# Kernel optimization log

Measured on AMD Instinct MI355X. Metric: run time of the kernel, lower is better.

Reference implementation:

```python
import jax, jax.numpy as jnp
import numpy as np

NODE_DIM = 128
OUT_DIM = 64
N_NODES = 50000
N_EDGES = 800000
NEG_SLOPE = 0.01  # F.leaky_relu default


def setup_inputs() -> dict:
    key = jax.random.key(0)
    k1, k2, k3, k4, k5 = jax.random.split(key, 5)
    h = jax.random.normal(k1, (N_NODES, NODE_DIM), dtype=jnp.float32)
    src = jax.random.randint(k2, (N_EDGES,), 0, N_NODES, dtype=jnp.int32)
    dst = jax.random.randint(k3, (N_EDGES,), 0, N_NODES, dtype=jnp.int32)
    # fc: Linear(node_dim, out_dim, bias=False); attn_fc: Linear(2*out_dim, 1, bias=False)
    W_fc = jax.random.normal(k4, (NODE_DIM, OUT_DIM), dtype=jnp.float32) * (1.0 / np.sqrt(NODE_DIM))
    W_attn = jax.random.normal(k5, (2 * OUT_DIM, 1), dtype=jnp.float32) * (1.0 / np.sqrt(2 * OUT_DIM))
    return {"h": h, "src": src, "dst": dst, "W_fc": W_fc, "W_attn": W_attn}


def reference(h, src, dst, W_fc, W_attn):
    N = h.shape[0]
    D = W_fc.shape[1]
    z = h @ W_fc                                   # [N, D]
    # attn_fc(concat(z_src, z_dst)) == z_src @ Wa[:D] + z_dst @ Wa[D:]
    s_src = (z @ W_attn[:D]).squeeze(-1)            # [N]
    s_dst = (z @ W_attn[D:]).squeeze(-1)            # [N]
    e = jax.nn.leaky_relu(s_src[src] + s_dst[dst], NEG_SLOPE)  # [E]
    # segment softmax over incoming edges per dst node
    m = jax.ops.segment_max(e, dst, num_segments=N)            # [N]
    ex = jnp.exp(e - m[dst])                                   # [E]
    denom = jax.ops.segment_sum(ex, dst, num_segments=N)       # [N]
    alpha = ex / denom[dst]                                    # [E]
    # weighted scatter-sum of src features into dst nodes
    out = jax.ops.segment_sum(alpha[:, None] * z[src], dst, num_segments=N)  # [N, D]
    return out
```

## Files before the change

kernel.cpp:

```cpp
#include <hip/hip_runtime.h>

#define NODE_DIM 128
#define OUT_DIM  64
#define NEG_SLOPE 0.01f
#define EPB   4096
#define CAPC  64
#define MAXB  4800

typedef __attribute__((ext_vector_type(8))) short short8;
typedef __attribute__((ext_vector_type(4))) short short4v;
typedef __attribute__((ext_vector_type(4))) float float4e;

__device__ __forceinline__ unsigned short f2bf(float f) {
    unsigned u = __float_as_uint(f);
    unsigned r = (u + 0x7FFFu + ((u >> 16) & 1u)) >> 16;
    return (unsigned short)r;
}
__device__ __forceinline__ float bf2f(unsigned short v) {
    return __uint_as_float((unsigned)v << 16);
}
__device__ __forceinline__ void split_bf(float v, short& hi, short& lo) {
    unsigned short h = f2bf(v);
    float r = v - bf2f(h);
    hi = (short)h;
    lo = (short)f2bf(r);
}

__global__ __launch_bounds__(256) void k_proj_part(
    const float* __restrict__ h, const float* __restrict__ Wf,
    const float* __restrict__ Wa,
    unsigned short* __restrict__ zbf,
    float* __restrict__ s_src, float* __restrict__ s_dst,
    const int* __restrict__ src, const int* __restrict__ dst,
    int* __restrict__ chunks, int* __restrict__ bhist,
    int N, int E, int PB, int nblkP)
{
    if (blockIdx.x >= (unsigned)PB) {
        __shared__ int cnt[256];
        const int blk = blockIdx.x - PB;
        const int t = threadIdx.x;
        cnt[t] = 0;
        __syncthreads();
        const int e0 = blk * EPB + t * 16;
        if (e0 < E) {
            int ne = E - e0; if (ne > 16) ne = 16;
            if (ne == 16) {
                int db[16], sb[16];
                const int4* dp = (const int4*)(dst + e0);
                const int4* sp = (const int4*)(src + e0);
                #pragma unroll
                for (int q = 0; q < 4; ++q) {
                    int4 dv = dp[q], svv = sp[q];
                    db[q*4+0]=dv.x; db[q*4+1]=dv.y; db[q*4+2]=dv.z; db[q*4+3]=dv.w;
                    sb[q*4+0]=svv.x; sb[q*4+1]=svv.y; sb[q*4+2]=svv.z; sb[q*4+3]=svv.w;
                }
                #pragma unroll
                for (int k = 0; k < 16; ++k) {
                    int d = db[k];
                    int bk = d >> 8;
                    int r = atomicAdd(&cnt[bk], 1);
                    if (r < CAPC)
                        chunks[((size_t)bk * nblkP + blk) * CAPC + r] = ((d & 255) << 17) | sb[k];
                }
            } else {
                for (int k = 0; k < ne; ++k) {
                    int d = dst[e0 + k];
                    int bk = d >> 8;
                    int r = atomicAdd(&cnt[bk], 1);
                    if (r < CAPC)
                        chunks[((size_t)bk * nblkP + blk) * CAPC + r] = ((d & 255) << 17) | src[e0 + k];
                }
            }
        }
        __syncthreads();
        bhist[t * nblkP + blk] = (cnt[t] < CAPC) ? cnt[t] : CAPC;
        return;
    }
    const int t    = threadIdx.x;
    const int wv   = t >> 6;
    const int lane = t & 63;
    const int m    = lane & 15;
    const int quad = lane >> 4;
    const int row0 = blockIdx.x * 64 + wv * 16;

    int rowc = row0 + m; if (rowc > N - 1) rowc = N - 1;
    const float* hrow = h + (size_t)rowc * NODE_DIM;
    short8 Ahi[4], Alo[4];
    #pragma unroll
    for (int t4 = 0; t4 < 4; ++t4) {
        float4e v0 = *(const float4e*)(hrow + t4 * 32 + quad * 8);
        float4e v1 = *(const float4e*)(hrow + t4 * 32 + quad * 8 + 4);
        #pragma unroll
        for (int j = 0; j < 4; ++j) {
            short hi, lo;
            split_bf(v0[j], hi, lo);
            Ahi[t4][j] = hi; Alo[t4][j] = lo;
            split_bf(v1[j], hi, lo);
            Ahi[t4][4 + j] = hi; Alo[t4][4 + j] = lo;
        }
    }

    float ps[4] = {0.f, 0.f, 0.f, 0.f};
    float pd[4] = {0.f, 0.f, 0.f, 0.f};

    #pragma unroll
    for (int c = 0; c < 4; ++c) {
        float4e acc = {0.f, 0.f, 0.f, 0.f};
        int col = c * 16 + m;
        #pragma unroll
        for (int t4 = 0; t4 < 4; ++t4) {
            short8 bh, bl;
            #pragma unroll
            for (int j = 0; j < 8; ++j) {
                short hi, lo;
                split_bf(Wf[(t4 * 32 + quad * 8 + j) * OUT_DIM + col], hi, lo);
                bh[j] = hi; bl[j] = lo;
            }
            acc = __builtin_amdgcn_mfma_f32_16x16x32_bf16(Alo[t4], bh, acc, 0, 0, 0);
            acc = __builtin_amdgcn_mfma_f32_16x16x32_bf16(Ahi[t4], bl, acc, 0, 0, 0);
            acc = __builtin_amdgcn_mfma_f32_16x16x32_bf16(Ahi[t4], bh, acc, 0, 0, 0);
        }
        float was = Wa[col];
        float wad = Wa[OUT_DIM + col];
        #pragma unroll
        for (int r = 0; r < 4; ++r) {
            int nrow = row0 + quad * 4 + r;
            if (nrow < N) zbf[(size_t)nrow * OUT_DIM + col] = f2bf(acc[r]);
            ps[r] = fmaf(acc[r], was, ps[r]);
            pd[r] = fmaf(acc[r], wad, pd[r]);
        }
    }

    #pragma unroll
    for (int r = 0; r < 4; ++r) {
        #pragma unroll
        for (int off = 1; off < 16; off <<= 1) {
            ps[r] += __shfl_xor(ps[r], off, 64);
            pd[r] += __shfl_xor(pd[r], off, 64);
        }
    }
    if (m == 0) {
        #pragma unroll
        for (int r = 0; r < 4; ++r) {
            int nrow = row0 + quad * 4 + r;
            if (nrow < N) { s_src[nrow] = ps[r]; s_dst[nrow] = pd[r]; }
        }
    }
}

__global__ __launch_bounds__(1024) void k_bucket_agg(
    const int* __restrict__ chunks, const int* __restrict__ bhist,
    const float* __restrict__ s_src, const float* __restrict__ s_dst,
    const unsigned short* __restrict__ zbf,
    float* __restrict__ out, int N, int nblkP)
{
    __shared__ int soff[257];
    __shared__ int sU[MAXB];
    __shared__ int sSrc[MAXB];
    __shared__ float xs[MAXB];
    __shared__ int cntN[256], curN[256], rsN[256], sscan[256];
    const int b = blockIdx.x;
    const int t = threadIdx.x;

    int v = 0;
    if (t < 256) {
        v = (t < nblkP) ? bhist[b * nblkP + t] : 0;
        sscan[t] = v;
        cntN[t] = 0;
    }
    __syncthreads();
    #pragma unroll
    for (int off = 1; off < 256; off <<= 1) {
        int u = 0;
        if (t < 256 && t >= off) u = sscan[t - off];
        __syncthreads();
        if (t < 256) sscan[t] += u;
        __syncthreads();
    }
    if (t < 256) soff[t] = sscan[t] - v;
    if (t == 255) soff[256] = sscan[255];
    __syncthreads();
    int total = soff[256];
    if (total > MAXB) total = MAXB;

    for (int i = t; i < total; i += 1024) {
        int lo = 0, hi = nblkP;
        while (hi - lo > 1) {
            int mid = (lo + hi) >> 1;
            if (soff[mid] <= i) lo = mid; else hi = mid;
        }
        int val = chunks[((size_t)b * nblkP + lo) * CAPC + (i - soff[lo])];
        sU[i] = val;
        atomicAdd(&cntN[val >> 17], 1);
    }
    __syncthreads();
    int vc = 0;
    if (t < 256) { vc = cntN[t]; sscan[t] = vc; }
    __syncthreads();
    #pragma unroll
    for (int off = 1; off < 256; off <<= 1) {
        int u = 0;
        if (t < 256 && t >= off) u = sscan[t - off];
        __syncthreads();
        if (t < 256) sscan[t] += u;
        __syncthreads();
    }
    if (t < 256) { rsN[t] = sscan[t] - vc; curN[t] = sscan[t] - vc; }
    __syncthreads();
    const int nodeBase = b * 256;
    for (int i = t; i < total; i += 1024) {
        int val = sU[i];
        int n8 = val >> 17;
        int sidx = val & 0x1FFFF;
        int pos = atomicAdd(&curN[n8], 1);
        sSrc[pos] = sidx;
        float e = s_src[sidx] + s_dst[nodeBase + n8];
        e = (e > 0.f) ? e : e * NEG_SLOPE;
        xs[pos] = __expf(e);
    }
    __syncthreads();

    const int wid = t >> 6, lane = t & 63;
    const int quad = lane >> 4, col4 = (lane & 15) * 4;
    for (int k = 0; k < 16; ++k) {
        int n8 = wid * 16 + k;
        int node = nodeBase + n8;
        if (node >= N) continue;
        int rs = rsN[n8], dg = cntN[n8];
        if (dg == 0) {
            if (quad == 0) {
                float4e o = {0.f, 0.f, 0.f, 0.f};
                *(float4e*)(out + (size_t)node * OUT_DIM + col4) = o;
            }
            continue;
        }
        float a0 = 0.f, a1 = 0.f, a2 = 0.f, a3 = 0.f, den = 0.f;
        for (int base = 0; base < dg; base += 64)
            if (lane < dg - base) den += xs[rs + base + lane];
        for (int j = 0; j < dg; j += 16) {
            #pragma unroll
            for (int g = 0; g < 4; ++g) {
                int ei = j + g * 4 + quad;
                int idx = rs + ((ei < dg) ? ei : 0);
                int ss = sSrc[idx];
                float xx = (ei < dg) ? xs[idx] : 0.f;
                short4v zv = *(const short4v*)(zbf + ((unsigned)ss << 6) + col4);
                a0 = fmaf(xx, bf2f((unsigned short)zv[0]), a0);
                a1 = fmaf(xx, bf2f((unsigned short)zv[1]), a1);
                a2 = fmaf(xx, bf2f((unsigned short)zv[2]), a2);
                a3 = fmaf(xx, bf2f((unsigned short)zv[3]), a3);
            }
        }
        a0 += __shfl_xor(a0, 16, 64); a0 += __shfl_xor(a0, 32, 64);
        a1 += __shfl_xor(a1, 16, 64); a1 += __shfl_xor(a1, 32, 64);
        a2 += __shfl_xor(a2, 16, 64); a2 += __shfl_xor(a2, 32, 64);
        a3 += __shfl_xor(a3, 16, 64); a3 += __shfl_xor(a3, 32, 64);
        #pragma unroll
        for (int off = 32; off > 0; off >>= 1) den += __shfl_xor(den, off, 64);
        if (quad == 0) {
            float4e o;
            o[0] = a0 / den; o[1] = a1 / den; o[2] = a2 / den; o[3] = a3 / den;
            *(float4e*)(out + (size_t)node * OUT_DIM + col4) = o;
        }
    }
}

extern "C" void kernel_launch(void* const* d_in, const int* in_sizes, int n_in,
                              void* d_out, int out_size, void* d_ws, size_t ws_size,
                              hipStream_t stream) {
    const float* h   = (const float*)d_in[0];
    const int*   src = (const int*)d_in[1];
    const int*   dst = (const int*)d_in[2];
    const float* Wf  = (const float*)d_in[3];
    const float* Wa  = (const float*)d_in[4];
    const int N = in_sizes[0] / NODE_DIM;
    const int E = in_sizes[1];
    float* out = (float*)d_out;

    const int PB    = (N + 63) / 64;
    const int nblkP = (E + EPB - 1) / EPB;
    const int nbB   = (N + 255) / 256;

    char* ws = (char*)d_ws;
    size_t off = 0;
    int* chunks = (int*)(ws + off);             off += (size_t)256 * nblkP * CAPC * sizeof(int);
    int* bhist  = (int*)(ws + off);             off += (size_t)256 * nblkP * sizeof(int);
    unsigned short* zbf = (unsigned short*)(ws + off); off += (size_t)N * OUT_DIM * sizeof(unsigned short);
    float* s_src = (float*)(ws + off);          off += (size_t)N * sizeof(float);
    float* s_dst = (float*)(ws + off);          off += (size_t)N * sizeof(float);

    k_proj_part<<<PB + nblkP, 256, 0, stream>>>(h, Wf, Wa, zbf, s_src, s_dst,
                                                src, dst, chunks, bhist, N, E, PB, nblkP);
    k_bucket_agg<<<nbB, 1024, 0, stream>>>(chunks, bhist, s_src, s_dst, zbf, out, N, nblkP);
}
```

Measured before the change: 133.2 us.

## Stage W split in LDS, coalesce z stores, restructure bucket aggregation

The projection kernel now splits W_fc into bf16 hi/lo parts once per block in shared memory, instead of having every wave reload and resplit it from global memory. It also stages z tiles through LDS so that global stores are coalesced 16-byte rows rather than scattered 2-byte writes. The aggregation kernel drops the binary-search compaction into sU and reads chunks directly per wave twice. It also assigns one node per 16-lane group, so each group walks its edges serially with 4-way unrolling and no cross-quad shuffles, which risks load imbalance across high-degree nodes.

```diff
diff --git a/kernel.cpp b/kernel.cpp
--- a/kernel.cpp
+++ b/kernel.cpp
@@ -35,8 +35,13 @@
     int* __restrict__ chunks, int* __restrict__ bhist,
     int N, int E, int PB, int nblkP)
 {
+    __shared__ union {
+        short w[16384];
+        unsigned short zt[4][16][68];
+    } uni;
+    __shared__ int cnt[256];
+
     if (blockIdx.x >= (unsigned)PB) {
-        __shared__ int cnt[256];
         const int blk = blockIdx.x - PB;
         const int t = threadIdx.x;
         cnt[t] = 0;
@@ -76,6 +81,7 @@
         bhist[t * nblkP + blk] = (cnt[t] < CAPC) ? cnt[t] : CAPC;
         return;
     }
+
     const int t    = threadIdx.x;
     const int wv   = t >> 6;
     const int lane = t & 63;
@@ -83,6 +89,26 @@
     const int quad = lane >> 4;
     const int row0 = blockIdx.x * 64 + wv * 16;
 
+    {
+        short* wh = uni.w;
+        short* wl = uni.w + 8192;
+        for (int s = t; s < 1024; s += 256) {
+            int combo = s >> 6;
+            int ln    = s & 63;
+            int c = combo >> 2, t4 = combo & 3;
+            int col = c * 16 + (ln & 15);
+            int kq  = t4 * 32 + (ln >> 4) * 8;
+            #pragma unroll
+            for (int j = 0; j < 8; ++j) {
+                short hi, lo;
+                split_bf(Wf[(kq + j) * OUT_DIM + col], hi, lo);
+                wh[s * 8 + j] = hi;
+                wl[s * 8 + j] = lo;
+            }
+        }
+    }
+    __syncthreads();
+
     int rowc = row0 + m; if (rowc > N - 1) rowc = N - 1;
     const float* hrow = h + (size_t)rowc * NODE_DIM;
     short8 Ahi[4], Alo[4];
@@ -102,30 +128,28 @@
 
     float ps[4] = {0.f, 0.f, 0.f, 0.f};
     float pd[4] = {0.f, 0.f, 0.f, 0.f};
-
+    unsigned short z16[16];
+
+    const short* wh = uni.w;
+    const short* wl = uni.w + 8192;
     #pragma unroll
     for (int c = 0; c < 4; ++c) {
         float4e acc = {0.f, 0.f, 0.f, 0.f};
-        int col = c * 16 + m;
         #pragma unroll
         for (int t4 = 0; t4 < 4; ++t4) {
-            short8 bh, bl;
-            #pragma unroll
-            for (int j = 0; j < 8; ++j) {
-                short hi, lo;
-                split_bf(Wf[(t4 * 32 + quad * 8 + j) * OUT_DIM + col], hi, lo);
-                bh[j] = hi; bl[j] = lo;
-            }
+            int slot = (c * 4 + t4) * 64 + lane;
+            short8 bh = *(const short8*)(wh + slot * 8);
+            short8 bl = *(const short8*)(wl + slot * 8);
             acc = __builtin_amdgcn_mfma_f32_16x16x32_bf16(Alo[t4], bh, acc, 0, 0, 0);
             acc = __builtin_amdgcn_mfma_f32_16x16x32_bf16(Ahi[t4], bl, acc, 0, 0, 0);
             acc = __builtin_amdgcn_mfma_f32_16x16x32_bf16(Ahi[t4], bh, acc, 0, 0, 0);
         }
+        int col = c * 16 + m;
         float was = Wa[col];
         float wad = Wa[OUT_DIM + col];
         #pragma unroll
         for (int r = 0; r < 4; ++r) {
-            int nrow = row0 + quad * 4 + r;
-            if (nrow < N) zbf[(size_t)nrow * OUT_DIM + col] = f2bf(acc[r]);
+            z16[c * 4 + r] = f2bf(acc[r]);
             ps[r] = fmaf(acc[r], was, ps[r]);
             pd[r] = fmaf(acc[r], wad, pd[r]);
         }
@@ -144,6 +168,26 @@
         for (int r = 0; r < 4; ++r) {
             int nrow = row0 + quad * 4 + r;
             if (nrow < N) { s_src[nrow] = ps[r]; s_dst[nrow] = pd[r]; }
+        }
+    }
+
+    __syncthreads();
+    {
+        unsigned short (*zt)[68] = uni.zt[wv];
+        #pragma unroll
+        for (int c = 0; c < 4; ++c)
+            #pragma unroll
+            for (int r = 0; r < 4; ++r)
+                zt[quad * 4 + r][c * 16 + m] = z16[c * 4 + r];
+        short* zb = (short*)zbf;
+        #pragma unroll
+        for (int i = 0; i < 2; ++i) {
+            int r    = i * 8 + (lane >> 3);
+            int colb = (lane & 7) * 8;
+            short8 zz = *(const short8*)&zt[r][colb];
+            int grow = row0 + r;
+            if (grow < N)
+                *(short8*)(zb + (size_t)grow * OUT_DIM + colb) = zz;
         }
     }
 }
@@ -154,20 +198,28 @@
     const unsigned short* __restrict__ zbf,
     float* __restrict__ out, int N, int nblkP)
 {
-    __shared__ int soff[257];
-    __shared__ int sU[MAXB];
-    __shared__ int sSrc[MAXB];
+    __shared__ int   sSrc[MAXB];
     __shared__ float xs[MAXB];
-    __shared__ int cntN[256], curN[256], rsN[256], sscan[256];
+    __shared__ int cntN[256], rsN[256], curN[256], sscan[256];
     const int b = blockIdx.x;
     const int t = threadIdx.x;
-
-    int v = 0;
-    if (t < 256) {
-        v = (t < nblkP) ? bhist[b * nblkP + t] : 0;
-        sscan[t] = v;
-        cntN[t] = 0;
-    }
+    const int wid = t >> 6, lane = t & 63;
+    const int nodeBase = b * 256;
+
+    if (t < 256) cntN[t] = 0;
+    __syncthreads();
+
+    for (int c = wid; c < nblkP; c += 16) {
+        int cc = bhist[b * nblkP + c];
+        if (lane < cc) {
+            int val = chunks[((size_t)b * nblkP + c) * CAPC + lane];
+            atomicAdd(&cntN[val >> 17], 1);
+        }
+    }
+    __syncthreads();
+
+    int vc = 0;
+    if (t < 256) { vc = cntN[t]; sscan[t] = vc; }
     __syncthreads();
     #pragma unroll
     for (int off = 1; off < 256; off <<= 1) {
@@ -177,90 +229,79 @@
         if (t < 256) sscan[t] += u;
         __syncthreads();
     }
-    if (t < 256) soff[t] = sscan[t] - v;
-    if (t == 255) soff[256] = sscan[255];
-    __syncthreads();
-    int total = soff[256];
-    if (total > MAXB) total = MAXB;
-
-    for (int i = t; i < total; i += 1024) {
-        int lo = 0, hi = nblkP;
-        while (hi - lo > 1) {
-            int mid = (lo + hi) >> 1;
-            if (soff[mid] <= i) lo = mid; else hi = mid;
-        }
-        int val = chunks[((size_t)b * nblkP + lo) * CAPC + (i - soff[lo])];
-        sU[i] = val;
-        atomicAdd(&cntN[val >> 17], 1);
-    }
-    __syncthreads();
-    int vc = 0;
-    if (t < 256) { vc = cntN[t]; sscan[t] = vc; }
-    __syncthreads();
-    #pragma unroll
-    for (int off = 1; off < 256; off <<= 1) {
-        int u = 0;
-        if (t < 256 && t >= off) u = sscan[t - off];
-        __syncthreads();
-        if (t < 256) sscan[t] += u;
-        __syncthreads();
-    }
     if (t < 256) { rsN[t] = sscan[t] - vc; curN[t] = sscan[t] - vc; }
     __syncthreads();
-    const int nodeBase = b * 256;
-    for (int i = t; i < total; i += 1024) {
-        int val = sU[i];
-        int n8 = val >> 17;
-        int sidx = val & 0x1FFFF;
-        int pos = atomicAdd(&curN[n8], 1);
-        sSrc[pos] = sidx;
-        float e = s_src[sidx] + s_dst[nodeBase + n8];
-        e = (e > 0.f) ? e : e * NEG_SLOPE;
-        xs[pos] = __expf(e);
-    }
-    __syncthreads();
-
-    const int wid = t >> 6, lane = t & 63;
-    const int quad = lane >> 4, col4 = (lane & 15) * 4;
-    for (int k = 0; k < 16; ++k) {
-        int n8 = wid * 16 + k;
+
+    for (int c = wid; c < nblkP; c += 16) {
+        int cc = bhist[b * nblkP + c];
+        if (lane < cc) {
+            int val = chunks[((size_t)b * nblkP + c) * CAPC + lane];
+            int n8 = val >> 17;
+            int sidx = val & 0x1FFFF;
+            int pos = atomicAdd(&curN[n8], 1);
+            sSrc[pos] = sidx;
+            float e = s_src[sidx] + s_dst[nodeBase + n8];
+            e = (e > 0.f) ? e : e * NEG_SLOPE;
+            xs[pos] = __expf(e);
+        }
+    }
+    __syncthreads();
+
+    const short* zb = (const short*)zbf;
+    const int cl8 = (lane & 15) * 4;
+    #pragma unroll
+    for (int pass = 0; pass < 4; ++pass) {
+        int n8 = pass * 64 + wid * 4 + (lane >> 4);
         int node = nodeBase + n8;
-        if (node >= N) continue;
         int rs = rsN[n8], dg = cntN[n8];
-        if (dg == 0) {
-            if (quad == 0) {
-                float4e o = {0.f, 0.f, 0.f, 0.f};
-                *(float4e*)(out + (size_t)node * OUT_DIM + col4) = o;
+        float a0 = 0.f, a1 = 0.f, a2 = 0.f, a3 = 0.f, den = 0.f;
+        int e = 0;
+        for (; e + 4 <= dg; e += 4) {
+            int i0 = rs + e;
+            int ss0 = sSrc[i0], ss1 = sSrc[i0+1], ss2 = sSrc[i0+2], ss3 = sSrc[i0+3];
+            float x0 = xs[i0], x1 = xs[i0+1], x2 = xs[i0+2], x3 = xs[i0+3];
+            short4v z0 = *(const short4v*)(zb + ((size_t)(unsigned)ss0 << 6) + cl8);
+            short4v z1 = *(const short4v*)(zb + ((size_t)(unsigned)ss1 << 6) + cl8);
+            short4v z2 = *(const short4v*)(zb + ((size_t)(unsigned)ss2 << 6) + cl8);
+            short4v z3 = *(const short4v*)(zb + ((size_t)(unsigned)ss3 << 6) + cl8);
+            den += (x0 + x1) + (x2 + x3);
+            a0 = fmaf(x0, bf2f((unsigned short)z0[0]), a0);
+            a1 = fmaf(x0, bf2f((unsigned short)z0[1]), a1);
+            a2 = fmaf(x0, bf2f((unsigned short)z0[2]), a2);
+            a3 = fmaf(x0, bf2f((unsigned short)z0[3]), a3);
+            a0 = fmaf(x1, bf2f((unsigned short)z1[0]), a0);
+            a1 = fmaf(x1, bf2f((unsigned short)z1[1]), a1);
+            a2 = fmaf(x1, bf2f((unsigned short)z1[2]), a2);
+            a3 = fmaf(x1, bf2f((unsigned short)z1[3]), a3);
+            a0 = fmaf(x2, bf2f((unsigned short)z2[0]), a0);
+            a1 = fmaf(x2, bf2f((unsigned short)z2[1]), a1);
+            a2 = fmaf(x2, bf2f((unsigned short)z2[2]), a2);
+            a3 = fmaf(x2, bf2f((unsigned short)z2[3]), a3);
+            a0 = fmaf(x3, bf2f((unsigned short)z3[0]), a0);
+            a1 = fmaf(x3, bf2f((unsigned short)z3[1]), a1);
+            a2 = fmaf(x3, bf2f((unsigned short)z3[2]), a2);
+            a3 = fmaf(x3, bf2f((unsigned short)z3[3]), a3);
+        }
+        for (; e < dg; ++e) {
+            int i0 = rs + e;
+            int ss0 = sSrc[i0];
+            float x0 = xs[i0];
+            short4v z0 = *(const short4v*)(zb + ((size_t)(unsigned)ss0 << 6) + cl8);
+            den += x0;
+            a0 = fmaf(x0, bf2f((unsigned short)z0[0]), a0);
+            a1 = fmaf(x0, bf2f((unsigned short)z0[1]), a1);
+            a2 = fmaf(x0, bf2f((unsigned short)z0[2]), a2);
+            a3 = fmaf(x0, bf2f((unsigned short)z0[3]), a3);
+        }
+        if (node < N) {
+            float4e o;
+            if (dg > 0) {
+                float inv = 1.f / den;
+                o[0] = a0 * inv; o[1] = a1 * inv; o[2] = a2 * inv; o[3] = a3 * inv;
+            } else {
+                o[0] = 0.f; o[1] = 0.f; o[2] = 0.f; o[3] = 0.f;
             }
-            continue;
-        }
-        float a0 = 0.f, a1 = 0.f, a2 = 0.f, a3 = 0.f, den = 0.f;
-        for (int base = 0; base < dg; base += 64)
-            if (lane < dg - base) den += xs[rs + base + lane];
-        for (int j = 0; j < dg; j += 16) {
-            #pragma unroll
-            for (int g = 0; g < 4; ++g) {
-                int ei = j + g * 4 + quad;
-                int idx = rs + ((ei < dg) ? ei : 0);
-                int ss = sSrc[idx];
-                float xx = (ei < dg) ? xs[idx] : 0.f;
-                short4v zv = *(const short4v*)(zbf + ((unsigned)ss << 6) + col4);
-                a0 = fmaf(xx, bf2f((unsigned short)zv[0]), a0);
-                a1 = fmaf(xx, bf2f((unsigned short)zv[1]), a1);
-                a2 = fmaf(xx, bf2f((unsigned short)zv[2]), a2);
-                a3 = fmaf(xx, bf2f((unsigned short)zv[3]), a3);
-            }
-        }
-        a0 += __shfl_xor(a0, 16, 64); a0 += __shfl_xor(a0, 32, 64);
-        a1 += __shfl_xor(a1, 16, 64); a1 += __shfl_xor(a1, 32, 64);
-        a2 += __shfl_xor(a2, 16, 64); a2 += __shfl_xor(a2, 32, 64);
-        a3 += __shfl_xor(a3, 16, 64); a3 += __shfl_xor(a3, 32, 64);
-        #pragma unroll
-        for (int off = 32; off > 0; off >>= 1) den += __shfl_xor(den, off, 64);
-        if (quad == 0) {
-            float4e o;
-            o[0] = a0 / den; o[1] = a1 / den; o[2] = a2 / den; o[3] = a3 / den;
-            *(float4e*)(out + (size_t)node * OUT_DIM + col4) = o;
+            *(float4e*)(out + (size_t)node * OUT_DIM + cl8) = o;
         }
     }
 }
```

Measured after the change: 119.8 us. 1.11x faster.
